# Kernel optimization log

Measured on AMD Instinct MI355X. Metric: run time of the kernel, lower is better.

Reference implementation:

```python
import jax, jax.numpy as jnp
import numpy as np

PI = 3.14159  # matches the literal in the torch source


def _grid_sample_border(img, gx, gy):
    """Bilinear grid_sample, align_corners=False, padding_mode='border'.
    img: (N, H, W); gx, gy: (N, H, W) normalized coords in [-1, 1]."""
    N, H, W = img.shape
    # unnormalize (align_corners=False) then clamp to image (border padding)
    x = jnp.clip(((gx + 1.0) * W - 1.0) * 0.5, 0.0, W - 1.0)
    y = jnp.clip(((gy + 1.0) * H - 1.0) * 0.5, 0.0, H - 1.0)
    x0f = jnp.floor(x)
    y0f = jnp.floor(y)
    wx = x - x0f
    wy = y - y0f
    x0 = jnp.clip(x0f.astype(jnp.int32), 0, W - 1)
    y0 = jnp.clip(y0f.astype(jnp.int32), 0, H - 1)
    x1 = jnp.clip(x0 + 1, 0, W - 1)
    y1 = jnp.clip(y0 + 1, 0, H - 1)
    flat = img.reshape(N, H * W)

    def gather(yi, xi):
        idx = (yi * W + xi).reshape(N, H * W)
        return jnp.take_along_axis(flat, idx, axis=1).reshape(N, H, W)

    v00 = gather(y0, x0)
    v01 = gather(y0, x1)
    v10 = gather(y1, x0)
    v11 = gather(y1, x1)
    return (v00 * (1 - wx) * (1 - wy) + v01 * wx * (1 - wy)
            + v10 * (1 - wx) * wy + v11 * wx * wy)


def setup_inputs() -> dict:
    key = jax.random.key(0)
    ks = jax.random.split(key, 8)
    B, D, H, W = 8, 256, 128, 128
    para_ch, feature_ch = 256, 256
    s = 0.05
    return {
        "feature_map": jax.random.normal(ks[0], (B, D, H, W), dtype=jnp.float32),
        "para_code": jax.random.normal(ks[1], (B, para_ch), dtype=jnp.float32),
        "W1": jax.random.normal(ks[2], (para_ch, para_ch), dtype=jnp.float32) * s,
        "b1": jnp.zeros((para_ch,), dtype=jnp.float32),
        "Ws": jax.random.normal(ks[3], (para_ch, feature_ch), dtype=jnp.float32) * s,
        "bs": jnp.zeros((feature_ch,), dtype=jnp.float32),
        "Wr": jax.random.normal(ks[4], (para_ch, feature_ch), dtype=jnp.float32) * s,
        "br": jnp.zeros((feature_ch,), dtype=jnp.float32),
        "Wt": jax.random.normal(ks[5], (para_ch, 2 * feature_ch), dtype=jnp.float32) * s,
        "bt": jnp.zeros((2 * feature_ch,), dtype=jnp.float32),
    }


def reference(feature_map, para_code, W1, b1, Ws, bs, Wr, br, Wt, bt):
    B, D, H, W = feature_map.shape
    p = jax.nn.relu(para_code @ W1 + b1)                      # (B, para_ch)
    scale = jax.nn.sigmoid(p @ Ws + bs) * 2.0                 # (B, D)
    angle = jnp.tanh(p @ Wr + br) * PI                        # (B, D)
    trans = jnp.tanh(p @ Wt + bt).reshape(B, D, 2)            # (B, D, 2)

    dt = feature_map.dtype
    gx = (2.0 * jnp.arange(W, dtype=dt) / (W - 1) - 1.0)[None, :]   # (1, W)
    gy = (2.0 * jnp.arange(H, dtype=dt) / (H - 1) - 1.0)[:, None]   # (H, 1)

    c = jnp.cos(angle)[:, :, None, None]                      # (B, D, 1, 1)
    s = jnp.sin(angle)[:, :, None, None]
    sc = scale[:, :, None, None]
    # R @ [x; y] = [c*x - s*y, s*x + c*y], then * scale + translation
    new_x = (c * gx - s * gy) * sc + trans[:, :, 0][:, :, None, None]  # (B,D,H,W)
    new_y = (s * gx + c * gy) * sc + trans[:, :, 1][:, :, None, None]

    out = _grid_sample_border(feature_map.reshape(B * D, H, W),
                              new_x.reshape(B * D, H, W),
                              new_y.reshape(B * D, H, W))
    return out.reshape(B, D, H, W)
```

## Files before the change

kernel.cpp:

```cpp
#include <hip/hip_runtime.h>
#include <math.h>


#define B_  8
#define D_  256
#define H_  128
#define W_  128
#define PC_ 256
#define PI_F 3.14159f
#define LPU_ 130

__global__ __launch_bounds__(1024)
void k_p(const float* __restrict__ para, const float* __restrict__ W1,
         const float* __restrict__ b1, float* __restrict__ p_out) {
    __shared__ float red[1024];
    const int b = blockIdx.x;
    const int t = threadIdx.x;
    const int d = t & 255;
    const int kc = t >> 8;
    float acc = 0.0f;
#pragma unroll 8
    for (int i = 0; i < 64; ++i) {
        const int k = kc * 64 + i;
        acc = fmaf(para[b * PC_ + k], W1[k * PC_ + d], acc);
    }
    red[t] = acc;
    __syncthreads();
    if (t < 256) {
        const float v = red[t] + red[t + 256] + red[t + 512] + red[t + 768] + b1[t];
        p_out[b * PC_ + t] = fmaxf(v, 0.0f);
    }
}

__global__ __launch_bounds__(512, 8)
void k_sample(const float* __restrict__ fm,
              const float* __restrict__ p_ws,
              const float* __restrict__ Ws, const float* __restrict__ bs,
              const float* __restrict__ Wr, const float* __restrict__ br,
              const float* __restrict__ Wt, const float* __restrict__ bt,
              float* __restrict__ out) {
    __shared__ unsigned short lds[129 * LPU_];
    __shared__ float red[8];

    const int plane = blockIdx.x;
    const int b = plane >> 8;
    const int d = plane & 255;
    const float* __restrict__ img = fm + (size_t)plane * (H_ * W_);
    float* __restrict__ op = out + (size_t)plane * (H_ * W_);
    const int tid = threadIdx.x;
    const int lane = tid & 63;
    const int wid = tid >> 6;

    float dp;
    {
        const int q = tid >> 7;
        const int kh = tid & 127;
        const float2 pk = ((const float2*)(p_ws + b * PC_))[kh];
        const float* __restrict__ Wq = (q == 0) ? Ws : (q == 1) ? Wr : Wt;
        const int stride = (q < 2) ? PC_ : 2 * PC_;
        const int col = (q < 2) ? d : (2 * d + (q & 1));
        const int k0 = kh * 2;
        dp = pk.x * Wq[k0 * stride + col] + pk.y * Wq[(k0 + 1) * stride + col];
    }

    {
        const float4* __restrict__ src = (const float4*)img;
#pragma unroll
        for (int j = 0; j < 8; ++j) {
            const int e4 = j * 512 + tid;
            const float4 v = src[e4];
            const int h = e4 >> 5;
            const int w = (e4 & 31) * 4;
            unsigned int lo, hi;
            {
                unsigned int ux = __float_as_uint(v.x); ux += 0x7FFFu + ((ux >> 16) & 1u);
                unsigned int uy = __float_as_uint(v.y); uy += 0x7FFFu + ((uy >> 16) & 1u);
                unsigned int uz = __float_as_uint(v.z); uz += 0x7FFFu + ((uz >> 16) & 1u);
                unsigned int uw = __float_as_uint(v.w); uw += 0x7FFFu + ((uw >> 16) & 1u);
                lo = (ux >> 16) | (uy & 0xFFFF0000u);
                hi = (uz >> 16) | (uw & 0xFFFF0000u);
            }
            unsigned int* dst = (unsigned int*)&lds[h * LPU_ + w];
            dst[0] = lo;
            dst[1] = hi;
        }
    }
    if (tid < H_ + 1)  lds[tid * LPU_ + W_] = 0;
    if (tid < LPU_)    lds[H_ * LPU_ + tid] = 0;

#pragma unroll
    for (int off = 32; off > 0; off >>= 1) dp += __shfl_down(dp, off);
    if (lane == 0) red[wid] = dp;

    __syncthreads();

    const float as_ = red[0] + red[1] + bs[d];
    const float ar_ = red[2] + red[3] + br[d];
    const float t0_ = red[4] + red[5] + bt[2 * d];
    const float t1_ = red[6] + red[7] + bt[2 * d + 1];
    const float sc = 2.0f / (1.0f + expf(-as_));
    const float ang = tanhf(ar_) * PI_F;
    const float cc = cosf(ang);
    const float ss = sinf(ang);
    const float tx = tanhf(t0_);
    const float ty = tanhf(t1_);

    const float gstep = 2.0f / (float)(W_ - 1);
    const float k64 = (float)W_ * 0.5f;
    const float ax =  cc * sc * gstep * k64;
    const float bx = -ss * sc * gstep * k64;
    const float cx = (tx - cc * sc + ss * sc + 1.0f) * k64 - 0.5f;
    const float ay =  ss * sc * gstep * k64;
    const float by =  cc * sc * gstep * k64;
    const float cy = (ty - ss * sc - cc * sc + 1.0f) * k64 - 0.5f;

    const int h0 = tid >> 7;
    const int w0 = tid & (W_ - 1);
    const float xb = fmaf((float)w0, ax, fmaf((float)h0, bx, cx));
    const float yb = fmaf((float)w0, ay, fmaf((float)h0, by, cy));
    const float dx4 = 4.0f * bx;
    const float dy4 = 4.0f * by;

#pragma unroll
    for (int b4 = 0; b4 < 8; ++b4) {
        float wxv[4], wyv[4];
        unsigned short t00[4], t01[4], t10[4], t11[4];

#pragma unroll
        for (int u = 0; u < 4; ++u) {
            const float it = (float)(b4 * 4 + u);
            float x = fmaf(it, dx4, xb);
            float y = fmaf(it, dy4, yb);
            x = fminf(fmaxf(x, 0.0f), (float)(W_ - 1));
            y = fminf(fmaxf(y, 0.0f), (float)(H_ - 1));
            const float x0f = floorf(x);
            const float y0f = floorf(y);
            wxv[u] = x - x0f;
            wyv[u] = y - y0f;
            const int base = (int)fmaf(y0f, (float)LPU_, x0f);
            t00[u] = lds[base];
            t01[u] = lds[base + 1];
            t10[u] = lds[base + LPU_];
            t11[u] = lds[base + LPU_ + 1];
        }

        __builtin_amdgcn_sched_barrier(0);

#pragma unroll
        for (int u = 0; u < 4; ++u) {
            const float v00 = __uint_as_float((unsigned int)t00[u] << 16);
            const float v01 = __uint_as_float((unsigned int)t01[u] << 16);
            const float v10 = __uint_as_float((unsigned int)t10[u] << 16);
            const float v11 = __uint_as_float((unsigned int)t11[u] << 16);
            const int px = (b4 * 4 + u) * 512 + tid;
            const float top = v00 + wxv[u] * (v01 - v00);
            const float bot = v10 + wxv[u] * (v11 - v10);
            op[px] = top + wyv[u] * (bot - top);
        }
    }
}

extern "C" void kernel_launch(void* const* d_in, const int* in_sizes, int n_in,
                              void* d_out, int out_size, void* d_ws, size_t ws_size,
                              hipStream_t stream) {
    const float* feature_map = (const float*)d_in[0];
    const float* para_code   = (const float*)d_in[1];
    const float* W1 = (const float*)d_in[2];
    const float* b1 = (const float*)d_in[3];
    const float* Ws = (const float*)d_in[4];
    const float* bs = (const float*)d_in[5];
    const float* Wr = (const float*)d_in[6];
    const float* br = (const float*)d_in[7];
    const float* Wt = (const float*)d_in[8];
    const float* bt = (const float*)d_in[9];
    float* out = (float*)d_out;

    float* p_ws = (float*)d_ws;

    k_p<<<B_, 1024, 0, stream>>>(para_code, W1, b1, p_ws);
    k_sample<<<B_ * D_, 512, 0, stream>>>(feature_map, p_ws,
                                          Ws, bs, Wr, br, Wt, bt, out);
}
```

Measured before the change: 66.61 us.

## Fuse first MLP layer into sampling kernel, recomputing it per plane

```diff
diff --git a/kernel.cpp b/kernel.cpp
--- a/kernel.cpp
+++ b/kernel.cpp
@@ -10,36 +10,16 @@
 #define PI_F 3.14159f
 #define LPU_ 130
 
-__global__ __launch_bounds__(1024)
-void k_p(const float* __restrict__ para, const float* __restrict__ W1,
-         const float* __restrict__ b1, float* __restrict__ p_out) {
-    __shared__ float red[1024];
-    const int b = blockIdx.x;
-    const int t = threadIdx.x;
-    const int d = t & 255;
-    const int kc = t >> 8;
-    float acc = 0.0f;
-#pragma unroll 8
-    for (int i = 0; i < 64; ++i) {
-        const int k = kc * 64 + i;
-        acc = fmaf(para[b * PC_ + k], W1[k * PC_ + d], acc);
-    }
-    red[t] = acc;
-    __syncthreads();
-    if (t < 256) {
-        const float v = red[t] + red[t + 256] + red[t + 512] + red[t + 768] + b1[t];
-        p_out[b * PC_ + t] = fmaxf(v, 0.0f);
-    }
-}
-
 __global__ __launch_bounds__(512, 8)
-void k_sample(const float* __restrict__ fm,
-              const float* __restrict__ p_ws,
-              const float* __restrict__ Ws, const float* __restrict__ bs,
-              const float* __restrict__ Wr, const float* __restrict__ br,
-              const float* __restrict__ Wt, const float* __restrict__ bt,
-              float* __restrict__ out) {
+void k_fused(const float* __restrict__ fm,
+             const float* __restrict__ para,
+             const float* __restrict__ W1, const float* __restrict__ b1,
+             const float* __restrict__ Ws, const float* __restrict__ bs,
+             const float* __restrict__ Wr, const float* __restrict__ br,
+             const float* __restrict__ Wt, const float* __restrict__ bt,
+             float* __restrict__ out) {
     __shared__ unsigned short lds[129 * LPU_];
+    __shared__ float pred[512];
     __shared__ float red[8];
 
     const int plane = blockIdx.x;
@@ -51,16 +31,30 @@
     const int lane = tid & 63;
     const int wid = tid >> 6;
 
-    float dp;
+    const int q = tid >> 7;
+    const int kh = tid & 127;
+    const float* __restrict__ Wq = (q == 0) ? Ws : (q == 1) ? Wr : Wt;
+    const int stride = (q < 2) ? PC_ : 2 * PC_;
+    const int col = (q < 2) ? d : (2 * d + (q & 1));
+    const float w0 = Wq[(kh * 2) * stride + col];
+    const float w1 = Wq[(kh * 2 + 1) * stride + col];
+    const float2 b1p = ((const float2*)b1)[kh];
+    const float bs_v = bs[d];
+    const float br_v = br[d];
+    const float bt0 = bt[2 * d];
+    const float bt1 = bt[2 * d + 1];
+
     {
-        const int q = tid >> 7;
-        const int kh = tid & 127;
-        const float2 pk = ((const float2*)(p_ws + b * PC_))[kh];
-        const float* __restrict__ Wq = (q == 0) ? Ws : (q == 1) ? Wr : Wt;
-        const int stride = (q < 2) ? PC_ : 2 * PC_;
-        const int col = (q < 2) ? d : (2 * d + (q & 1));
-        const int k0 = kh * 2;
-        dp = pk.x * Wq[k0 * stride + col] + pk.y * Wq[(k0 + 1) * stride + col];
+        const int pd = tid & 255;
+        const int half = tid >> 8;
+        const float* __restrict__ pr = para + b * PC_ + half * 128;
+        const float* __restrict__ Wc = W1 + (half * 128) * PC_ + pd;
+        float acc = 0.0f;
+#pragma unroll 8
+        for (int i = 0; i < 128; ++i) {
+            acc = fmaf(pr[i], Wc[i * PC_], acc);
+        }
+        pred[tid] = acc;
     }
 
     {
@@ -88,16 +82,23 @@
     if (tid < H_ + 1)  lds[tid * LPU_ + W_] = 0;
     if (tid < LPU_)    lds[H_ * LPU_ + tid] = 0;
 
-#pragma unroll
-    for (int off = 32; off > 0; off >>= 1) dp += __shfl_down(dp, off);
-    if (lane == 0) red[wid] = dp;
-
     __syncthreads();
 
-    const float as_ = red[0] + red[1] + bs[d];
-    const float ar_ = red[2] + red[3] + br[d];
-    const float t0_ = red[4] + red[5] + bt[2 * d];
-    const float t1_ = red[6] + red[7] + bt[2 * d + 1];
+    {
+        const int k0 = kh * 2;
+        const float pa = fmaxf(pred[k0]     + pred[k0 + 256] + b1p.x, 0.0f);
+        const float pb = fmaxf(pred[k0 + 1] + pred[k0 + 257] + b1p.y, 0.0f);
+        float dp = pa * w0 + pb * w1;
+#pragma unroll
+        for (int off = 32; off > 0; off >>= 1) dp += __shfl_down(dp, off);
+        if (lane == 0) red[wid] = dp;
+    }
+    __syncthreads();
+
+    const float as_ = red[0] + red[1] + bs_v;
+    const float ar_ = red[2] + red[3] + br_v;
+    const float t0_ = red[4] + red[5] + bt0;
+    const float t1_ = red[6] + red[7] + bt1;
     const float sc = 2.0f / (1.0f + expf(-as_));
     const float ang = tanhf(ar_) * PI_F;
     const float cc = cosf(ang);
@@ -115,9 +116,9 @@
     const float cy = (ty - ss * sc - cc * sc + 1.0f) * k64 - 0.5f;
 
     const int h0 = tid >> 7;
-    const int w0 = tid & (W_ - 1);
-    const float xb = fmaf((float)w0, ax, fmaf((float)h0, bx, cx));
-    const float yb = fmaf((float)w0, ay, fmaf((float)h0, by, cy));
+    const int w0p = tid & (W_ - 1);
+    const float xb = fmaf((float)w0p, ax, fmaf((float)h0, bx, cx));
+    const float yb = fmaf((float)w0p, ay, fmaf((float)h0, by, cy));
     const float dx4 = 4.0f * bx;
     const float dy4 = 4.0f * by;
 
@@ -175,9 +176,6 @@
     const float* bt = (const float*)d_in[9];
     float* out = (float*)d_out;
 
-    float* p_ws = (float*)d_ws;
-
-    k_p<<<B_, 1024, 0, stream>>>(para_code, W1, b1, p_ws);
-    k_sample<<<B_ * D_, 512, 0, stream>>>(feature_map, p_ws,
-                                          Ws, bs, Wr, br, Wt, bt, out);
+    k_fused<<<B_ * D_, 512, 0, stream>>>(feature_map, para_code,
+                                         W1, b1, Ws, bs, Wr, br, Wt, bt, out);
 }
```

After: 74.82 us. 1.12x slower.
